# Optimization experiments

Hardware: AMD Instinct MI355X
Metric: run time of the kernel (lower is better)

Reference implementation:

```python
import jax, jax.numpy as jnp
import numpy as np

B, C, H, W = 4, 256, 64, 64
CI = 3
TEMPERATURE = 0.0001 * 5
EPS = 2.220446049250313e-16  # sys.float_info.epsilon


def _nearest_up4(x):
    # nn.Upsample(scale_factor=4, mode='nearest'): [B,C,H,W] -> [B,C,4H,4W]
    return jnp.repeat(jnp.repeat(x, 4, axis=2), 4, axis=3)


def _avg_pool2(x):
    # AvgPool2d(kernel=2, stride=2, pad=0)
    b, c, h, w = x.shape
    return x.reshape(b, c, h // 2, 2, w // 2, 2).mean(axis=(3, 5))


def _center_norm(feats):
    # subtract per-channel spatial mean, then L2-normalize over channels per position
    b, c, h, w = feats.shape
    t = feats.reshape(b, c, h * w)
    t = t - t.mean(axis=-1, keepdims=True)
    n = jnp.linalg.norm(t, axis=1, keepdims=True) + EPS
    return t / n  # [B,C,HW]


def setup_inputs() -> dict:
    key = jax.random.key(0)
    k1, k2, k3 = jax.random.split(key, 3)
    return {
        "x_feats": jax.random.normal(k1, (B, C, H, W), jnp.float32),
        "y_feats": jax.random.normal(k2, (B, C, H, W), jnp.float32),
        "y_img": jax.random.uniform(k3, (B, CI, 4 * H, 4 * W), jnp.float32),
    }


def reference(x_feats, y_feats, y_img):
    b, c, h, w = x_feats.shape
    hw = h * w
    theta = _center_norm(x_feats)  # [B,C,HW]
    phi = _center_norm(y_feats)    # [B,C,HW]
    f = jnp.einsum('bcm,bcn->bmn', theta, phi)  # dense correlation [B,HW,HW]
    loss_feat_pair = jnp.mean(jnp.abs(theta - phi))  # F.l1_loss(theta, phi)
    # WTA_scale_weight == 1 -> WTA branch bypassed, just temperature scaling
    f_wta = f / TEMPERATURE
    f_div_c = jax.nn.softmax(f_wta, axis=-1)  # [B,HW,HW]
    # warped features: f_div_C @ y_feats^T
    b_lab = y_feats.reshape(b, c, hw)
    y = jnp.einsum('bmn,bcn->bcm', f_div_c, b_lab).reshape(b, c, h, w)
    # soft-argmax coordinates
    xc = (jnp.arange(hw) % w).astype(x_feats.dtype)   # [HW]
    yc = (jnp.arange(hw) // w).astype(x_feats.dtype)  # [HW]
    coords_x = f_div_c @ xc  # [B,HW]
    coords_y = f_div_c @ yc  # [B,HW]
    coords1 = jnp.stack([coords_x, coords_y], axis=1).reshape(b, 2, h, w)
    coords0 = jnp.stack([xc, yc], axis=0).reshape(1, 2, h, w)
    flow = _nearest_up4(coords1 - coords0)  # [B,2,4H,4W]
    # image warping branch (y_img is not None)
    yi = _avg_pool2(_avg_pool2(y_img))  # [B,CI,H,W]
    ci = yi.shape[1]
    yi_flat = yi.reshape(b, ci, hw)
    y_img_attn = jnp.einsum('bmn,bcn->bmc', f_div_c, yi_flat)  # [B,HW,CI]
    f_div_c_v = jax.nn.softmax(jnp.swapaxes(f_wta, 1, 2), axis=-1)
    y_img_cyc = jnp.einsum('bmn,bnc->bcm', f_div_c_v, y_img_attn).reshape(b, ci, h, w)
    y_img_out = jnp.swapaxes(y_img_attn, 1, 2).reshape(b, ci, h, w)
    return (y, flow, _nearest_up4(y_img_out), _nearest_up4(y_img_cyc), loss_feat_pair)
```

## Files before the change

kernel.cpp:

```cpp
#include <hip/hip_runtime.h>
#include <math.h>

#define HW   4096
#define NCH  256
#define NB   4

constexpr float TEMP  = (float)(0.0001 * 5.0);
constexpr float INV_T = 1.0f / TEMP;
constexpr float EPSN  = 2.220446049250313e-16f;

typedef __attribute__((ext_vector_type(8))) _Float16 f16x8;
typedef __attribute__((ext_vector_type(4))) _Float16 f16x4;
typedef __attribute__((ext_vector_type(4))) float    f32x4;

constexpr size_t OFF_YT    = 0;
constexpr size_t OFF_YI    = OFF_YT    + (size_t)NB*HW*NCH;
constexpr size_t OFF_MEAN  = OFF_YI    + (size_t)NB*3*HW;
constexpr size_t OFF_RNORM = OFF_MEAN  + (size_t)2*NB*NCH;
constexpr size_t OFF_NSQP  = OFF_RNORM + (size_t)2*NB*HW;
constexpr size_t OFF_F     = OFF_NSQP  + (size_t)2*NB*8*HW;
constexpr size_t OFF_ZUP   = OFF_F     + (size_t)HW*HW/2;
constexpr size_t OFF_CYCP  = OFF_ZUP;
constexpr size_t OFF_ROWP  = OFF_CYCP  + (size_t)NB*32*4*HW;
constexpr size_t OFF_COLP  = OFF_ROWP  + (size_t)32*7*HW;
constexpr size_t OFF_YP    = OFF_F     + (size_t)HW*HW;
constexpr size_t OFF_RMAX  = OFF_YP    + (size_t)8*NCH*HW;
constexpr size_t OFF_RSUM  = OFF_RMAX  + HW;
constexpr size_t OFF_CMAX  = OFF_RSUM  + (size_t)NB*HW;
constexpr size_t OFF_RMB   = OFF_CMAX  + HW;
constexpr size_t OFF_COORD = OFF_RMB   + (size_t)32*HW;
constexpr size_t OFF_ATTN  = OFF_COORD + (size_t)NB*2*HW;
constexpr size_t OFF_CYC   = OFF_ATTN  + (size_t)NB*HW*3;
constexpr size_t OFF_LOSSP = OFF_CYC   + (size_t)NB*3*HW;
constexpr size_t OFF_F16   = OFF_LOSSP + 1024;

constexpr size_t OUT_Y    = 0;
constexpr size_t OUT_FLOW = (size_t)NB*NCH*HW;
constexpr size_t OUT_IMG  = OUT_FLOW + (size_t)NB*2*256*256;
constexpr size_t OUT_CYCO = OUT_IMG  + (size_t)NB*3*256*256;
constexpr size_t OUT_LOSS = OUT_CYCO + (size_t)NB*3*256*256;

__device__ __forceinline__ void gload16(const void* g, void* l) {
    __builtin_amdgcn_global_load_lds(
        (const __attribute__((address_space(1))) unsigned int*)g,
        (__attribute__((address_space(3))) unsigned int*)l, 16, 0, 0);
}

__global__ void mean_kernel(const float* __restrict__ xf, const float* __restrict__ yf,
                            float* __restrict__ means) {
    const float* src = (blockIdx.y == 0 ? xf : yf) + (size_t)blockIdx.x * HW;
    float s = 0.f;
    for (int i = threadIdx.x; i < HW; i += 256) s += src[i];
    __shared__ float red[256];
    red[threadIdx.x] = s; __syncthreads();
    for (int st = 128; st > 0; st >>= 1) {
        if (threadIdx.x < st) red[threadIdx.x] += red[threadIdx.x + st];
        __syncthreads();
    }
    if (threadIdx.x == 0) means[blockIdx.y * (NB*NCH) + blockIdx.x] = red[0] * (1.0f / HW);
}

__global__ void nsq_combine_kernel(const float* __restrict__ part, float* __restrict__ rnorms,
                                   int b) {
    int t = blockIdx.y;
    int m = blockIdx.x * 256 + threadIdx.x;
    const float* p = part + ((size_t)t*NB + b) * 8 * HW + m;
    float s = 0.f;
    for (int k = 0; k < 8; ++k) s += p[(size_t)k * HW];
    rnorms[((size_t)t*NB + b) * HW + m] = 1.0f / (sqrtf(s) + EPSN);
}

__global__ void ycast_kernel(const float* __restrict__ yf, _Float16* __restrict__ yf16) {
    size_t i = ((size_t)blockIdx.x * 256 + threadIdx.x) * 8;
    const float4* s = (const float4*)(yf + i);
    float4 v0 = s[0], v1 = s[1];
    f16x8 o;
    o[0]=(_Float16)v0.x; o[1]=(_Float16)v0.y; o[2]=(_Float16)v0.z; o[3]=(_Float16)v0.w;
    o[4]=(_Float16)v1.x; o[5]=(_Float16)v1.y; o[6]=(_Float16)v1.z; o[7]=(_Float16)v1.w;
    *(f16x8*)(yf16 + i) = o;
}

__global__ void prep_kernel(const float* __restrict__ xf, const float* __restrict__ yf,
                            const float* __restrict__ means,
                            _Float16* __restrict__ th, _Float16* __restrict__ tl,
                            _Float16* __restrict__ ph, _Float16* __restrict__ pl,
                            float* __restrict__ nsqp, int b) {
    __shared__ float tile[32][33];
    __shared__ float sqr[8][33];
    int t = blockIdx.z;
    int c0 = blockIdx.x * 32, m0 = blockIdx.y * 32;
    const float* src = (t == 0 ? xf : yf) + (size_t)b * NCH * HW;
    const float* mn  = means + t * (NB*NCH) + b * NCH;
    int tx = threadIdx.x & 31, ty = threadIdx.x >> 5;
    float sq = 0.f;
    for (int i = ty; i < 32; i += 8) {
        float v = src[(size_t)(c0 + i) * HW + m0 + tx] - mn[c0 + i];
        tile[i][tx] = v;
        sq += v * v;
    }
    sqr[ty][tx] = sq;
    __syncthreads();
    _Float16* H = (t == 0 ? th : ph);
    _Float16* L = (t == 0 ? tl : pl);
    for (int i = ty; i < 32; i += 8) {
        float v = tile[tx][i];
        _Float16 h = (_Float16)v;
        _Float16 l = (_Float16)(v - (float)h);
        H[(size_t)(m0 + i)*NCH + c0 + tx] = h;
        L[(size_t)(m0 + i)*NCH + c0 + tx] = l;
    }
    if (ty == 0) {
        float s = 0.f;
        #pragma unroll
        for (int k = 0; k < 8; ++k) s += sqr[k][tx];
        nsqp[(((size_t)t*NB + b) * 8 + blockIdx.x) * HW + m0 + tx] = s;
    }
}

__global__ void avgpool_kernel(const float* __restrict__ yimg, float* __restrict__ yi) {
    size_t idx = (size_t)blockIdx.x * 256 + threadIdx.x;
    int m  = (int)(idx & (HW - 1));
    int bc = (int)(idx >> 12);
    int h = m >> 6, w = m & 63;
    const float* p = yimg + (size_t)bc * 65536 + (size_t)(h*4) * 256 + w*4;
    float s = 0.f;
    #pragma unroll
    for (int dy = 0; dy < 4; ++dy) {
        #pragma unroll
        for (int dx = 0; dx < 4; ++dx) s += p[dy*256 + dx];
    }
    yi[idx] = s * (1.0f/16.0f);
}

__global__ __launch_bounds__(512) void gemm_f_kernel(
        const _Float16* __restrict__ th, const _Float16* __restrict__ tl,
        const _Float16* __restrict__ ph, const _Float16* __restrict__ pl,
        const float* __restrict__ rnorms, const float* __restrict__ yi,
        _Float16* __restrict__ zh, float* __restrict__ rowp, float* __restrict__ colp,
        float* __restrict__ rmb, int b) {
    __shared__ char lds[2][4][8192];
    int tid  = threadIdx.x;
    int lane = tid & 63;
    int w = tid >> 6;
    int wm = w >> 2;
    int wn = w & 3;
    int m0 = blockIdx.y * 128, n0 = blockIdx.x * 128;

    int o0 = tid * 16;
    int r0 = o0 >> 6, s0 = (o0 >> 4) & 3, g0 = s0 ^ ((r0 >> 1) & 3);
    size_t ga0 = (size_t)(n0 + r0)*NCH + g0*8;
    size_t gb0 = (size_t)(m0 + r0)*NCH + g0*8;

    int fra = wm*64 + (lane & 15);
    int frb = wn*32 + (lane & 15);
    int ks  = lane >> 4;

    auto STAGE = [&](int buf, int k0) {
        gload16(ph + ga0 + k0, &lds[buf][0][o0]);
        gload16(pl + ga0 + k0, &lds[buf][1][o0]);
        gload16(th + gb0 + k0, &lds[buf][2][o0]);
        gload16(tl + gb0 + k0, &lds[buf][3][o0]);
    };

    f32x4 acc[4][2];
    #pragma unroll
    for (int i = 0; i < 4; ++i)
        #pragma unroll
        for (int j = 0; j < 2; ++j) acc[i][j] = (f32x4){0.f, 0.f, 0.f, 0.f};

    STAGE(0, 0);
    __syncthreads();
    int cur = 0;
    for (int kt = 0; kt < 8; ++kt) {
        if (kt < 7) STAGE(cur ^ 1, (kt + 1) * 32);

        f16x8 ah[4], al[4], bh[2], bl[2];
        #pragma unroll
        for (int i = 0; i < 4; ++i) {
            int rowa = fra + i*16;
            int offa = rowa*64 + ((ks ^ ((rowa >> 1) & 3)) << 4);
            ah[i] = *(const f16x8*)&lds[cur][0][offa];
            al[i] = *(const f16x8*)&lds[cur][1][offa];
        }
        #pragma unroll
        for (int j = 0; j < 2; ++j) {
            int rowb = frb + j*16;
            int offb = rowb*64 + ((ks ^ ((rowb >> 1) & 3)) << 4);
            bh[j] = *(const f16x8*)&lds[cur][2][offb];
            bl[j] = *(const f16x8*)&lds[cur][3][offb];
        }
        __builtin_amdgcn_s_setprio(1);
        #pragma unroll
        for (int i = 0; i < 4; ++i)
            #pragma unroll
            for (int j = 0; j < 2; ++j) {
                acc[i][j] = __builtin_amdgcn_mfma_f32_16x16x32_f16(ah[i], bh[j], acc[i][j], 0, 0, 0);
                acc[i][j] = __builtin_amdgcn_mfma_f32_16x16x32_f16(ah[i], bl[j], acc[i][j], 0, 0, 0);
                acc[i][j] = __builtin_amdgcn_mfma_f32_16x16x32_f16(al[i], bh[j], acc[i][j], 0, 0, 0);
            }
        __builtin_amdgcn_s_setprio(0);
        __syncthreads();
        cur ^= 1;
    }

    const float* rnx = rnorms + (size_t)b * HW;
    const float* rny = rnorms + (size_t)(NB + b) * HW;
    int mg[2];  float rxv[2];
    #pragma unroll
    for (int j = 0; j < 2; ++j) {
        mg[j] = m0 + wn*32 + j*16 + (lane & 15);
        rxv[j] = rnx[mg[j]];
    }
    int nl0 = wm*64 + (lane >> 4)*4;
    #pragma unroll
    for (int i = 0; i < 4; ++i)
        #pragma unroll
        for (int r = 0; r < 4; ++r) {
            float ry = rny[n0 + nl0 + i*16 + r];
            #pragma unroll
            for (int j = 0; j < 2; ++j) acc[i][j][r] *= rxv[j] * ry;
        }

    float* S     = (float*)&lds[0][0][0];
    float* rowm  = S;
    float* sums6 = S + 256;
    float* colm  = S + 1792;

    #pragma unroll
    for (int j = 0; j < 2; ++j) {
        float v = acc[0][j][0];
        #pragma unroll
        for (int i = 0; i < 4; ++i)
            #pragma unroll
            for (int r = 0; r < 4; ++r) v = fmaxf(v, acc[i][j][r]);
        v = fmaxf(v, __shfl_xor(v, 16));
        v = fmaxf(v, __shfl_xor(v, 32));
        if (lane < 16) rowm[wm*128 + wn*32 + j*16 + lane] = v;
    }
    #pragma unroll
    for (int i = 0; i < 4; ++i)
        #pragma unroll
        for (int r = 0; r < 4; ++r) {
            float v = fmaxf(acc[i][0][r], acc[i][1][r]);
            #pragma unroll
            for (int d = 1; d < 16; d <<= 1) v = fmaxf(v, __shfl_xor(v, d));
            if ((lane & 15) == 0) colm[wn*128 + nl0 + i*16 + r] = v;
        }
    __syncthreads();

    float bm[2];
    #pragma unroll
    for (int j = 0; j < 2; ++j) {
        int ml = wn*32 + j*16 + (lane & 15);
        bm[j] = fmaxf(rowm[ml], rowm[128 + ml]);
    }
    float a6[2][6];
    #pragma unroll
    for (int j = 0; j < 2; ++j)
        #pragma unroll
        for (int q = 0; q < 6; ++q) a6[j][q] = 0.f;
    const float* yib = yi + (size_t)b * 3 * HW;
    #pragma unroll
    for (int i = 0; i < 4; ++i) {
        f16x4 zq[2];
        #pragma unroll
        for (int r = 0; r < 4; ++r) {
            int ng = n0 + nl0 + i*16 + r;
            float xc = (float)(ng & 63), yc = (float)(ng >> 6);
            float y0 = yib[ng], y1 = yib[HW + ng], y2 = yib[2*HW + ng];
            #pragma unroll
            for (int j = 0; j < 2; ++j) {
                float z = (acc[i][j][r] - bm[j]) * INV_T;
                float e = __expf(z);
                zq[j][r] = (_Float16)z;
                a6[j][0] += e;      a6[j][1] += e*xc; a6[j][2] += e*yc;
                a6[j][3] += e*y0;   a6[j][4] += e*y1; a6[j][5] += e*y2;
            }
        }
        #pragma unroll
        for (int j = 0; j < 2; ++j)
            *(f16x4*)&zh[(size_t)mg[j]*HW + n0 + nl0 + i*16] = zq[j];
    }
    #pragma unroll
    for (int j = 0; j < 2; ++j)
        #pragma unroll
        for (int q = 0; q < 6; ++q) {
            float v = a6[j][q];
            v += __shfl_xor(v, 16);
            v += __shfl_xor(v, 32);
            if (lane < 16) sums6[(wm*128 + wn*32 + j*16 + lane)*6 + q] = v;
        }
    __syncthreads();

    if (tid < 128) {
        int ml = tid;
        float m2 = fmaxf(rowm[ml], rowm[128 + ml]);
        rowp[((size_t)blockIdx.x*7 + 0)*HW + m0 + ml] = m2;
        rmb[(size_t)blockIdx.x*HW + m0 + ml] = m2;
        #pragma unroll
        for (int q = 0; q < 6; ++q)
            rowp[((size_t)blockIdx.x*7 + 1 + q)*HW + m0 + ml] =
                sums6[ml*6 + q] + sums6[(128 + ml)*6 + q];
    } else if (tid < 256) {
        int nl = tid - 128;
        float c2 = fmaxf(fmaxf(colm[nl], colm[128 + nl]),
                         fmaxf(colm[256 + nl], colm[384 + nl]));
        colp[(size_t)blockIdx.y*HW + n0 + nl] = c2;
    }
}

__global__ void rowcol_combine_kernel(const float* __restrict__ rowp,
        const float* __restrict__ colp,
        float* __restrict__ rmax, float* __restrict__ rsuminv,
        float* __restrict__ coords, float* __restrict__ attn,
        float* __restrict__ cmax, int b) {
    int idx = blockIdx.x * 256 + threadIdx.x;
    if (blockIdx.y == 0) {
        int m = idx;
        float gm = -3.0e38f;
        for (int t = 0; t < 32; ++t) gm = fmaxf(gm, rowp[((size_t)t*7)*HW + m]);
        float S=0, CX=0, CY=0, A0=0, A1=0, A2=0;
        for (int t = 0; t < 32; ++t) {
            const float* p = rowp + (size_t)t*7*HW + m;
            float wgt = __expf((p[0] - gm) * INV_T);
            S  += p[1*HW] * wgt; CX += p[2*HW] * wgt; CY += p[3*HW] * wgt;
            A0 += p[4*HW] * wgt; A1 += p[5*HW] * wgt; A2 += p[6*HW] * wgt;
        }
        float inv = 1.0f / S;
        rmax[m] = gm; rsuminv[m] = inv;
        coords[((size_t)b*2 + 0)*HW + m] = CX * inv;
        coords[((size_t)b*2 + 1)*HW + m] = CY * inv;
        attn[((size_t)b*HW + m)*3 + 0] = A0 * inv;
        attn[((size_t)b*HW + m)*3 + 1] = A1 * inv;
        attn[((size_t)b*HW + m)*3 + 2] = A2 * inv;
    } else {
        int n = idx;
        float gm = -3.0e38f;
        for (int t = 0; t < 32; ++t) gm = fmaxf(gm, colp[(size_t)t*HW + n]);
        cmax[n] = gm;
    }
}

__global__ __launch_bounds__(512) void gemm_y_kernel(const _Float16* __restrict__ zh,
        const float* __restrict__ rmax, const float* __restrict__ rmb,
        const _Float16* __restrict__ yf16, _Float16* __restrict__ yph, int b) {
    __shared__ __align__(16) char ldsA[2][4096];
    __shared__ __align__(16) char ldsB[2][16384];
    int tid  = threadIdx.x;
    int lane = tid & 63;
    int w = tid >> 6, wm = w >> 2, wn = w & 3;
    int m0 = blockIdx.x * 64;
    int ks = blockIdx.y;
    const _Float16* Yb = yf16 + (size_t)b * NCH * HW;

    int ar = tid >> 3, kc = tid & 7;
    int aslot = kc >> 1, ahalf = kc & 1;
    int aoff = ar*64 + ((aslot ^ ((ar >> 1) & 3)) << 4) + ahalf*8;
    float gm = rmax[m0 + ar];
    const _Float16* zrow = zh + (size_t)(m0 + ar)*HW + kc*4;
    const float* rmbm = rmb + (m0 + ar);

    int o0 = tid*16, o1 = o0 + 8192;
    int br0 = o0 >> 6, bs0 = (o0 >> 4) & 3, bg0 = bs0 ^ ((br0 >> 1) & 3);
    int br1 = o1 >> 6, bs1 = (o1 >> 4) & 3, bg1 = bs1 ^ ((br1 >> 1) & 3);
    size_t gb0 = (size_t)br0*HW + bg0*8;
    size_t gb1 = (size_t)br1*HW + bg1*8;

    int fra = wm*32 + (lane & 15);
    int frb = wn*64 + (lane & 15);
    int kslot = lane >> 4;

    auto STAGEB = [&](int buf, int k0) {
        gload16(Yb + gb0 + k0, &ldsB[buf][o0]);
        gload16(Yb + gb1 + k0, &ldsB[buf][o1]);
    };
    auto WRITEA = [&](int buf, int k0) {
        float cf = __expf((rmbm[(size_t)(k0 >> 7)*HW] - gm) * INV_T);
        f16x4 zv = *(const f16x4*)(zrow + k0);
        f16x4 pk;
        pk[0] = (_Float16)(__expf((float)zv[0]) * cf);
        pk[1] = (_Float16)(__expf((float)zv[1]) * cf);
        pk[2] = (_Float16)(__expf((float)zv[2]) * cf);
        pk[3] = (_Float16)(__expf((float)zv[3]) * cf);
        *(f16x4*)&ldsA[buf][aoff] = pk;
    };

    f32x4 acc[2][4];
    #pragma unroll
    for (int i = 0; i < 2; ++i)
        #pragma unroll
        for (int j = 0; j < 4; ++j) acc[i][j] = (f32x4){0.f, 0.f, 0.f, 0.f};

    int kbase = ks * 1024;
    WRITEA(0, kbase);
    STAGEB(0, kbase);
    __syncthreads();
    int cur = 0;
    for (int s = 0; s < 32; ++s) {
        int k0 = kbase + s*32;
        if (s < 31) {
            STAGEB(cur ^ 1, k0 + 32);
            WRITEA(cur ^ 1, k0 + 32);
        }
        f16x8 af[2], bf[4];
        #pragma unroll
        for (int i = 0; i < 2; ++i) {
            int rowa = fra + i*16;
            af[i] = *(const f16x8*)&ldsA[cur][rowa*64 + ((kslot ^ ((rowa >> 1) & 3)) << 4)];
        }
        #pragma unroll
        for (int j = 0; j < 4; ++j) {
            int rowb = frb + j*16;
            bf[j] = *(const f16x8*)&ldsB[cur][rowb*64 + ((kslot ^ ((rowb >> 1) & 3)) << 4)];
        }
        __builtin_amdgcn_s_setprio(1);
        #pragma unroll
        for (int i = 0; i < 2; ++i)
            #pragma unroll
            for (int j = 0; j < 4; ++j)
                acc[i][j] = __builtin_amdgcn_mfma_f32_16x16x32_f16(af[i], bf[j], acc[i][j], 0, 0, 0);
        __builtin_amdgcn_s_setprio(0);
        __syncthreads();
        cur ^= 1;
    }

    #pragma unroll
    for (int i = 0; i < 2; ++i) {
        int m = m0 + wm*32 + i*16 + (lane >> 4) * 4;
        #pragma unroll
        for (int j = 0; j < 4; ++j) {
            int c = wn*64 + j*16 + (lane & 15);
            f16x4 v;
            #pragma unroll
            for (int r = 0; r < 4; ++r) v[r] = (_Float16)acc[i][j][r];
            *(f16x4*)(yph + ((size_t)ks*NCH + c)*HW + m) = v;
        }
    }
}

__global__ void ycombine_kernel(const _Float16* __restrict__ yph, const float* __restrict__ rsum,
                                float* __restrict__ out) {
    int b = blockIdx.y;
    size_t idx = (size_t)blockIdx.x * 256 + threadIdx.x;
    int m = (int)(idx & (HW - 1));
    const _Float16* yb = yph + (size_t)b*4*NCH*HW;
    float s = 0.f;
    #pragma unroll
    for (int k = 0; k < 4; ++k) s += (float)yb[(size_t)k*NCH*HW + idx];
    out[OUT_Y + (size_t)b*NCH*HW + idx] = s * rsum[(size_t)b*HW + m];
}

__global__ __launch_bounds__(256) void cyc_partial_kernel(const _Float16* __restrict__ zh,
        const float* __restrict__ cmax, const float* __restrict__ rmb,
        const float* __restrict__ attn, float* __restrict__ part, int b) {
    __shared__ float at[128*3];
    __shared__ float bmL[2][128];
    int i  = blockIdx.x * 256 + threadIdx.x;
    int j0 = blockIdx.y * 128;
    for (int k = threadIdx.x; k < 384; k += 256)
        at[k] = attn[((size_t)b*HW + j0)*3 + k];
    {
        int k = threadIdx.x;
        bmL[k >> 7][k & 127] = rmb[((size_t)(blockIdx.x*2 + (k >> 7)))*HW + j0 + (k & 127)];
    }
    __syncthreads();
    float cm = cmax[i];
    int tl = threadIdx.x >> 7;
    float a0=0, a1=0, a2=0, a3=0;
    for (int jj = 0; jj < 128; ++jj) {
        float z = (float)zh[(size_t)(j0+jj)*HW + i];
        float e = __expf(z + (bmL[tl][jj] - cm) * INV_T);
        a0 = fmaf(e, at[jj*3+0], a0);
        a1 = fmaf(e, at[jj*3+1], a1);
        a2 = fmaf(e, at[jj*3+2], a2);
        a3 += e;
    }
    part[((size_t)blockIdx.y*4 + 0)*HW + i] = a0;
    part[((size_t)blockIdx.y*4 + 1)*HW + i] = a1;
    part[((size_t)blockIdx.y*4 + 2)*HW + i] = a2;
    part[((size_t)blockIdx.y*4 + 3)*HW + i] = a3;
}

__global__ void cyc_combine_kernel(const float* __restrict__ cycp, float* __restrict__ cyc) {
    int b = blockIdx.z;
    const float* part = cycp + (size_t)b*32*4*HW;
    int i = blockIdx.x * 256 + threadIdx.x;
    int c = blockIdx.y;
    float s = 0.f, den = 0.f;
    for (int k = 0; k < 32; ++k) {
        s   += part[((size_t)k*4 + c)*HW + i];
        den += part[((size_t)k*4 + 3)*HW + i];
    }
    cyc[((size_t)b*3 + c)*HW + i] = s / den;
}

__global__ void flow_kernel(const float* __restrict__ coords, float* __restrict__ out) {
    size_t idx = (size_t)blockIdx.x * 256 + threadIdx.x;
    int x4 = (int)(idx & 255);
    int y4 = (int)((idx >> 8) & 255);
    int ch = (int)((idx >> 16) & 1);
    int b  = (int)(idx >> 17);
    int w = x4 >> 2, h = y4 >> 2;
    int m = h*64 + w;
    float c1 = coords[((size_t)b*2 + ch)*HW + m];
    float c0 = (ch == 0) ? (float)w : (float)h;
    out[OUT_FLOW + idx] = c1 - c0;
}

__global__ void imgout_kernel(const float* __restrict__ attn, const float* __restrict__ cyc,
                              float* __restrict__ out) {
    size_t idx = (size_t)blockIdx.x * 256 + threadIdx.x;
    int x4 = (int)(idx & 255);
    int y4 = (int)((idx >> 8) & 255);
    int rest = (int)(idx >> 16);
    int ch = rest % 3, b = rest / 3;
    int m = (y4 >> 2)*64 + (x4 >> 2);
    out[OUT_IMG  + idx] = attn[((size_t)b*HW + m)*3 + ch];
    out[OUT_CYCO + idx] = cyc[((size_t)b*3 + ch)*HW + m];
}

__global__ void loss_partial_kernel(const float* __restrict__ xf, const float* __restrict__ yf,
                                    const float* __restrict__ means, const float* __restrict__ rnorms,
                                    float* __restrict__ part) {
    __shared__ float red[256];
    size_t base = (size_t)blockIdx.x * 4096;
    float s = 0.f;
    for (int k = 0; k < 16; ++k) {
        size_t id = base + (size_t)k*256 + threadIdx.x;
        int m  = (int)(id & (HW - 1));
        int bc = (int)(id >> 12);
        int b  = bc >> 8;
        float th = (xf[id] - means[bc])          * rnorms[(size_t)b*HW + m];
        float ph = (yf[id] - means[NB*NCH + bc]) * rnorms[(size_t)(NB + b)*HW + m];
        s += fabsf(th - ph);
    }
    red[threadIdx.x] = s; __syncthreads();
    for (int st = 128; st > 0; st >>= 1) {
        if (threadIdx.x < st) red[threadIdx.x] += red[threadIdx.x + st];
        __syncthreads();
    }
    if (threadIdx.x == 0) part[blockIdx.x] = red[0];
}

__global__ void loss_final_kernel(const float* __restrict__ part, float* __restrict__ out) {
    __shared__ float red[256];
    float s = 0.f;
    for (int k = threadIdx.x; k < 1024; k += 256) s += part[k];
    red[threadIdx.x] = s; __syncthreads();
    for (int st = 128; st > 0; st >>= 1) {
        if (threadIdx.x < st) red[threadIdx.x] += red[threadIdx.x + st];
        __syncthreads();
    }
    if (threadIdx.x == 0) out[OUT_LOSS] = red[0] * (1.0f / 4194304.0f);
}

extern "C" void kernel_launch(void* const* d_in, const int* in_sizes, int n_in,
                              void* d_out, int out_size, void* d_ws, size_t ws_size,
                              hipStream_t stream) {
    (void)in_sizes; (void)n_in; (void)out_size; (void)ws_size;
    const float* xf   = (const float*)d_in[0];
    const float* yf   = (const float*)d_in[1];
    const float* yimg = (const float*)d_in[2];
    float* out = (float*)d_out;
    float* ws  = (float*)d_ws;

    _Float16* yf16 = (_Float16*)(ws + OFF_YT);
    float* yi      = ws + OFF_YI;
    float* means   = ws + OFF_MEAN;
    float* rnorms  = ws + OFF_RNORM;
    float* nsqp    = ws + OFF_NSQP;
    _Float16* zh   = (_Float16*)(ws + OFF_F);
    _Float16* yph  = (_Float16*)(ws + OFF_YP);
    float* cycp    = ws + OFF_CYCP;
    float* rowp    = ws + OFF_ROWP;
    float* colp    = ws + OFF_COLP;
    float* rmax    = ws + OFF_RMAX;
    float* rsum    = ws + OFF_RSUM;
    float* cmax    = ws + OFF_CMAX;
    float* rmb     = ws + OFF_RMB;
    float* coords  = ws + OFF_COORD;
    float* attn    = ws + OFF_ATTN;
    float* cyc     = ws + OFF_CYC;
    float* lossp   = ws + OFF_LOSSP;
    _Float16* th = (_Float16*)(ws + OFF_F16);
    _Float16* tl = th + (size_t)HW*NCH;
    _Float16* ph = tl + (size_t)HW*NCH;
    _Float16* pl = ph + (size_t)HW*NCH;

    mean_kernel        <<<dim3(NB*NCH, 2),   256, 0, stream>>>(xf, yf, means);
    ycast_kernel       <<<2048,              256, 0, stream>>>(yf, yf16);
    avgpool_kernel     <<<NB*3*HW/256,       256, 0, stream>>>(yimg, yi);

    for (int b = 0; b < NB; ++b) {
        prep_kernel          <<<dim3(8, 128, 2), 256, 0, stream>>>(xf, yf, means, th, tl, ph, pl,
                                                                   nsqp, b);
        nsq_combine_kernel   <<<dim3(16, 2),     256, 0, stream>>>(nsqp, rnorms, b);
        gemm_f_kernel        <<<dim3(32, 32),    512, 0, stream>>>(th, tl, ph, pl, rnorms, yi,
                                                                   zh, rowp, colp, rmb, b);
        rowcol_combine_kernel<<<dim3(16, 2),     256, 0, stream>>>(rowp, colp, rmax,
                                                                   rsum + (size_t)b*HW,
                                                                   coords, attn, cmax, b);
        gemm_y_kernel        <<<dim3(64, 4),     512, 0, stream>>>(zh, rmax, rmb, yf16,
                                                                   yph + (size_t)b*4*NCH*HW, b);
        cyc_partial_kernel   <<<dim3(16, 32),    256, 0, stream>>>(zh, cmax, rmb, attn,
                                                                   cycp + (size_t)b*32*4*HW, b);
    }

    ycombine_kernel    <<<dim3(NCH*HW/256, NB), 256, 0, stream>>>(yph, rsum, out);
    cyc_combine_kernel <<<dim3(16, 3, NB),      256, 0, stream>>>(cycp, cyc);
    flow_kernel        <<<NB*2*65536/256, 256, 0, stream>>>(coords, out);
    imgout_kernel      <<<NB*3*65536/256, 256, 0, stream>>>(attn, cyc, out);
    loss_partial_kernel<<<1024,           256, 0, stream>>>(xf, yf, means, rnorms, lossp);
    loss_final_kernel  <<<1,              256, 0, stream>>>(lossp, out);
}
```

Before: 477.7 us.

## Hoist per-batch prep out of loop and swizzle GEMM block order for XCD locality

```diff
diff --git a/kernel.cpp b/kernel.cpp
--- a/kernel.cpp
+++ b/kernel.cpp
@@ -14,6 +14,7 @@
 typedef __attribute__((ext_vector_type(4))) float    f32x4;
 
 constexpr size_t OFF_YT    = 0;
+constexpr size_t OFF_PREP1 = OFF_YT    + (size_t)2097152;
 constexpr size_t OFF_YI    = OFF_YT    + (size_t)NB*HW*NCH;
 constexpr size_t OFF_MEAN  = OFF_YI    + (size_t)NB*3*HW;
 constexpr size_t OFF_RNORM = OFF_MEAN  + (size_t)2*NB*NCH;
@@ -23,6 +24,8 @@
 constexpr size_t OFF_CYCP  = OFF_ZUP;
 constexpr size_t OFF_ROWP  = OFF_CYCP  + (size_t)NB*32*4*HW;
 constexpr size_t OFF_COLP  = OFF_ROWP  + (size_t)32*7*HW;
+constexpr size_t OFF_PREP2 = OFF_COLP  + (size_t)32*HW;
+constexpr size_t OFF_PREP3 = OFF_PREP2 + (size_t)2097152;
 constexpr size_t OFF_YP    = OFF_F     + (size_t)HW*HW;
 constexpr size_t OFF_RMAX  = OFF_YP    + (size_t)8*NCH*HW;
 constexpr size_t OFF_RSUM  = OFF_RMAX  + HW;
@@ -60,9 +63,8 @@
     if (threadIdx.x == 0) means[blockIdx.y * (NB*NCH) + blockIdx.x] = red[0] * (1.0f / HW);
 }
 
-__global__ void nsq_combine_kernel(const float* __restrict__ part, float* __restrict__ rnorms,
-                                   int b) {
-    int t = blockIdx.y;
+__global__ void nsq_combine_kernel(const float* __restrict__ part, float* __restrict__ rnorms) {
+    int t = blockIdx.y, b = blockIdx.z;
     int m = blockIdx.x * 256 + threadIdx.x;
     const float* p = part + ((size_t)t*NB + b) * 8 * HW + m;
     float s = 0.f;
@@ -144,7 +146,12 @@
     int w = tid >> 6;
     int wm = w >> 2;
     int wn = w & 3;
-    int m0 = blockIdx.y * 128, n0 = blockIdx.x * 128;
+
+    int lid = blockIdx.y * 32 + blockIdx.x;
+    int xcd = lid & 7, kk = lid >> 3;
+    int bx = (xcd & 3) * 8 + (kk & 7);
+    int by = (xcd >> 2) * 16 + (kk >> 3);
+    int m0 = by * 128, n0 = bx * 128;
 
     int o0 = tid * 16;
     int r0 = o0 >> 6, s0 = (o0 >> 4) & 3, g0 = s0 ^ ((r0 >> 1) & 3);
@@ -295,17 +302,17 @@
     if (tid < 128) {
         int ml = tid;
         float m2 = fmaxf(rowm[ml], rowm[128 + ml]);
-        rowp[((size_t)blockIdx.x*7 + 0)*HW + m0 + ml] = m2;
-        rmb[(size_t)blockIdx.x*HW + m0 + ml] = m2;
+        rowp[((size_t)bx*7 + 0)*HW + m0 + ml] = m2;
+        rmb[(size_t)bx*HW + m0 + ml] = m2;
         #pragma unroll
         for (int q = 0; q < 6; ++q)
-            rowp[((size_t)blockIdx.x*7 + 1 + q)*HW + m0 + ml] =
+            rowp[((size_t)bx*7 + 1 + q)*HW + m0 + ml] =
                 sums6[ml*6 + q] + sums6[(128 + ml)*6 + q];
     } else if (tid < 256) {
         int nl = tid - 128;
         float c2 = fmaxf(fmaxf(colm[nl], colm[128 + nl]),
                          fmaxf(colm[256 + nl], colm[384 + nl]));
-        colp[(size_t)blockIdx.y*HW + n0 + nl] = c2;
+        colp[(size_t)by*HW + n0 + nl] = c2;
     }
 }
 
@@ -349,8 +356,11 @@
     int tid  = threadIdx.x;
     int lane = tid & 63;
     int w = tid >> 6, wm = w >> 2, wn = w & 3;
-    int m0 = blockIdx.x * 64;
-    int ks = blockIdx.y;
+
+    int lid = blockIdx.y * 64 + blockIdx.x;
+    int swz = (lid & 7) * 32 + (lid >> 3);
+    int mtile = swz & 63, ks = swz >> 6;
+    int m0 = mtile * 64;
     const _Float16* Yb = yf16 + (size_t)b * NCH * HW;
 
     int ar = tid >> 3, kc = tid & 7;
@@ -582,19 +592,28 @@
     float* attn    = ws + OFF_ATTN;
     float* cyc     = ws + OFF_CYC;
     float* lossp   = ws + OFF_LOSSP;
-    _Float16* th = (_Float16*)(ws + OFF_F16);
-    _Float16* tl = th + (size_t)HW*NCH;
-    _Float16* ph = tl + (size_t)HW*NCH;
-    _Float16* pl = ph + (size_t)HW*NCH;
+
+    const size_t prep_off[NB] = { OFF_F16, OFF_PREP1, OFF_PREP2, OFF_PREP3 };
 
     mean_kernel        <<<dim3(NB*NCH, 2),   256, 0, stream>>>(xf, yf, means);
     ycast_kernel       <<<2048,              256, 0, stream>>>(yf, yf16);
     avgpool_kernel     <<<NB*3*HW/256,       256, 0, stream>>>(yimg, yi);
 
     for (int b = 0; b < NB; ++b) {
-        prep_kernel          <<<dim3(8, 128, 2), 256, 0, stream>>>(xf, yf, means, th, tl, ph, pl,
-                                                                   nsqp, b);
-        nsq_combine_kernel   <<<dim3(16, 2),     256, 0, stream>>>(nsqp, rnorms, b);
+        _Float16* th = (_Float16*)(ws + prep_off[b]);
+        _Float16* tl = th + (size_t)HW*NCH;
+        _Float16* ph = tl + (size_t)HW*NCH;
+        _Float16* pl = ph + (size_t)HW*NCH;
+        prep_kernel    <<<dim3(8, 128, 2), 256, 0, stream>>>(xf, yf, means, th, tl, ph, pl,
+                                                             nsqp, b);
+    }
+    nsq_combine_kernel <<<dim3(16, 2, NB), 256, 0, stream>>>(nsqp, rnorms);
+
+    for (int b = 0; b < NB; ++b) {
+        _Float16* th = (_Float16*)(ws + prep_off[b]);
+        _Float16* tl = th + (size_t)HW*NCH;
+        _Float16* ph = tl + (size_t)HW*NCH;
+        _Float16* pl = ph + (size_t)HW*NCH;
         gemm_f_kernel        <<<dim3(32, 32),    512, 0, stream>>>(th, tl, ph, pl, rnorms, yi,
                                                                    zh, rowp, colp, rmb, b);
         rowcol_combine_kernel<<<dim3(16, 2),     256, 0, stream>>>(rowp, colp, rmax,
```

New measurement: 469.8 us, median of 2. Within noise of the previous version (-1.6%).
